# Kernel optimization log

Hardware: AMD Instinct MI355X
Metric: run time of the kernel (lower is better)

Reference implementation:

```python
import jax, jax.numpy as jnp
import numpy as np

D_IN = 1024
D_OUT = 1024
B, S = 4, 2048

def setup_inputs() -> dict:
    key = jax.random.key(0)
    ks = jax.random.split(key, 7)
    s_in = 1.0 / np.sqrt(D_IN)
    return {
        "X": jax.random.normal(ks[0], (B, S, D_IN), dtype=jnp.float32),
        "Wq": jax.random.uniform(ks[1], (D_OUT, D_IN), jnp.float32, -s_in, s_in),
        "bq": jax.random.uniform(ks[2], (D_OUT,), jnp.float32, -s_in, s_in),
        "Wk": jax.random.uniform(ks[3], (D_OUT, D_IN), jnp.float32, -s_in, s_in),
        "bk": jax.random.uniform(ks[4], (D_OUT,), jnp.float32, -s_in, s_in),
        "Wv": jax.random.uniform(ks[5], (D_OUT, D_IN), jnp.float32, -s_in, s_in),
        "bv": jax.random.uniform(ks[6], (D_OUT,), jnp.float32, -s_in, s_in),
    }

def reference(X, Wq, bq, Wk, bk, Wv, bv):
    # Linear projections (torch Linear: x @ W.T + b)
    q = X @ Wq.T + bq            # [B, S, D_OUT]
    k = X @ Wk.T + bk
    v = X @ Wv.T + bv
    scores = jnp.einsum("bqd,bkd->bqk", q, k) / jnp.sqrt(jnp.float32(D_OUT))
    seq = scores.shape[-1]
    causal = jnp.tril(jnp.ones((seq, seq), dtype=bool))  # True where allowed
    scores = jnp.where(causal, scores, -jnp.inf)
    attn = jax.nn.softmax(scores, axis=-1)
    return jnp.einsum("bqk,bkd->bqd", attn, v)
```

## Files before the change

kernel.cpp:

```cpp
#include <hip/hip_runtime.h>
#include <hip/hip_bf16.h>


typedef __attribute__((ext_vector_type(8))) short short8;
typedef __attribute__((ext_vector_type(4))) float floatx4;

#define SEQ   2048
#define DMODEL 1024
#define NBATCH 4
#define MTOT  (SEQ * NBATCH)

__device__ __forceinline__ void stage16(const __hip_bfloat16* g, __hip_bfloat16* l)
{
  __builtin_amdgcn_global_load_lds(
      (const __attribute__((address_space(1))) void*)g,
      (__attribute__((address_space(3))) void*)l, 16, 0, 0);
}

__device__ __forceinline__ unsigned short bf16_bits(float f)
{
  __hip_bfloat16 h = __float2bfloat16(f);
  return *(unsigned short*)&h;
}

__global__ __launch_bounds__(256) void convert_all(
    const float* __restrict__ X,  const float* __restrict__ Wq,
    const float* __restrict__ Wk, const float* __restrict__ Wv,
    __hip_bfloat16* __restrict__ Xb,  __hip_bfloat16* __restrict__ Wqb,
    __hip_bfloat16* __restrict__ Wkb, __hip_bfloat16* __restrict__ Wvb)
{
  const int b = blockIdx.x;
  const float* src; __hip_bfloat16* dst; int rel;
  if (b < 8192)       { src = X;  dst = Xb;  rel = b; }
  else if (b < 9216)  { src = Wq; dst = Wqb; rel = b - 8192; }
  else if (b < 10240) { src = Wk; dst = Wkb; rel = b - 9216; }
  else                { src = Wv; dst = Wvb; rel = b - 10240; }
  const int i = rel * 1024 + threadIdx.x * 4;
  float4 f = *(const float4*)(src + i);
  uint2 o;
  o.x = (unsigned)bf16_bits(f.x) | ((unsigned)bf16_bits(f.y) << 16);
  o.y = (unsigned)bf16_bits(f.z) | ((unsigned)bf16_bits(f.w) << 16);
  *(uint2*)(dst + i) = o;
}

__global__ __launch_bounds__(256, 2) void gemm_qkv_fused(
    const __hip_bfloat16* __restrict__ Xb,
    const __hip_bfloat16* __restrict__ Wqb,
    const __hip_bfloat16* __restrict__ Wkb,
    const __hip_bfloat16* __restrict__ Wvb,
    const float* __restrict__ bq, const float* __restrict__ bk, const float* __restrict__ bv,
    __hip_bfloat16* __restrict__ Qb, __hip_bfloat16* __restrict__ Kb, __hip_bfloat16* __restrict__ Vt)
{
  __shared__ __hip_bfloat16 As[128 * 32];
  __shared__ __hip_bfloat16 Bs[3][128 * 32];
  const int m0 = blockIdx.y * 128, n0 = blockIdx.x * 128;
  const int tid  = threadIdx.x;
  const int lane = tid & 63;
  const int wave = tid >> 6;
  const int quad = lane >> 4;
  const int r    = lane & 15;
  const int wm   = (wave >> 1) * 64;
  const int wn   = (wave & 1) * 64;
  const int srow = wave * 16 + (lane >> 2);
  const int scol = (lane & 3) * 8;

  const __hip_bfloat16* Wp[3] = {Wqb, Wkb, Wvb};

  __hip_bfloat16* lA0 = As + wave * 512;
  __hip_bfloat16* lA1 = As + 2048 + wave * 512;

  const __hip_bfloat16* aR0 = Xb + (size_t)(m0 + srow) * DMODEL + scol;
  const __hip_bfloat16* aR1 = aR0 + (size_t)64 * DMODEL;

  floatx4 acc[3][4][4] = {};

  for (int kt = 0; kt < DMODEL / 32; ++kt) {
    const int k0 = kt * 32;
    stage16(aR0 + k0, lA0);
    stage16(aR1 + k0, lA1);
#pragma unroll
    for (int w = 0; w < 3; ++w) {
      stage16(Wp[w] + (size_t)(n0 + srow) * DMODEL + scol + k0,      Bs[w] + wave * 512);
      stage16(Wp[w] + (size_t)(n0 + 64 + srow) * DMODEL + scol + k0, Bs[w] + 2048 + wave * 512);
    }
    __syncthreads();
    short8 a[4];
#pragma unroll
    for (int i = 0; i < 4; ++i)
      a[i] = *(const short8*)(As + (wm + i * 16 + r) * 32 + quad * 8);
#pragma unroll
    for (int w = 0; w < 3; ++w) {
      short8 b[4];
#pragma unroll
      for (int j = 0; j < 4; ++j)
        b[j] = *(const short8*)(Bs[w] + (wn + j * 16 + r) * 32 + quad * 8);
#pragma unroll
      for (int i = 0; i < 4; ++i)
#pragma unroll
        for (int j = 0; j < 4; ++j)
          acc[w][i][j] = __builtin_amdgcn_mfma_f32_16x16x32_bf16(a[i], b[j], acc[w][i][j], 0, 0, 0);
    }
    __syncthreads();
  }

  {
    __hip_bfloat16* Op[2] = {Qb, Kb};
    const float* Bp[2] = {bq, bk};
#pragma unroll
    for (int w = 0; w < 2; ++w) {
      __hip_bfloat16* out = Op[w];
#pragma unroll
      for (int j = 0; j < 4; ++j) {
        const int n = n0 + wn + j * 16 + r;
        const float bb = Bp[w][n];
#pragma unroll
        for (int i = 0; i < 4; ++i) {
          const int mbase = m0 + wm + i * 16 + quad * 4;
#pragma unroll
          for (int e = 0; e < 4; ++e)
            out[(size_t)(mbase + e) * DMODEL + n] = __float2bfloat16(acc[w][i][j][e] + bb);
        }
      }
    }
  }
  {
    const int z    = m0 >> 11;
    const int posb = (m0 & (SEQ - 1)) + wm;
    __hip_bfloat16* vt = Vt + (size_t)z * DMODEL * SEQ;
#pragma unroll
    for (int j = 0; j < 4; ++j) {
      const int n = n0 + wn + j * 16 + r;
      const float bb = bv[n];
#pragma unroll
      for (int i = 0; i < 4; ++i) {
        const int pos = posb + i * 16 + quad * 4;
        unsigned long long pk =
            (unsigned long long)bf16_bits(acc[2][i][j][0] + bb)
          | ((unsigned long long)bf16_bits(acc[2][i][j][1] + bb) << 16)
          | ((unsigned long long)bf16_bits(acc[2][i][j][2] + bb) << 32)
          | ((unsigned long long)bf16_bits(acc[2][i][j][3] + bb) << 48);
        *(unsigned long long*)(vt + (size_t)n * SEQ + pos) = pk;
      }
    }
  }
}

__device__ __forceinline__ void gemm_core_2w(
    const __hip_bfloat16* __restrict__ A,
    const __hip_bfloat16* __restrict__ B,
    int K, int m0, int n0, int kchunks,
    __hip_bfloat16* As , __hip_bfloat16* Bs ,
    floatx4 acc[4][4])
{
  const int tid  = threadIdx.x;
  const int lane = tid & 63;
  const int wave = tid >> 6;
  const int quad = lane >> 4;
  const int r    = lane & 15;
  const int wn   = wave * 64;
  const int lrow = lane >> 2;
  const int lcol = (lane & 3) * 8;

  const __hip_bfloat16* aB = A + (size_t)(m0 + wave * 32 + lrow) * K + lcol;
  const __hip_bfloat16* bB = B + (size_t)(n0 + wave * 64 + lrow) * K + lcol;
  __hip_bfloat16* lA = As + wave * 1024;
  __hip_bfloat16* lB = Bs + wave * 2048;

  for (int kt = 0; kt < kchunks; ++kt) {
    const int k0 = kt * 32;
#pragma unroll
    for (int s = 0; s < 2; ++s)
      stage16(aB + (size_t)(16 * s) * K + k0, lA + s * 512);
#pragma unroll
    for (int s = 0; s < 4; ++s)
      stage16(bB + (size_t)(16 * s) * K + k0, lB + s * 512);
    __syncthreads();
    short8 a[4], b[4];
#pragma unroll
    for (int i = 0; i < 4; ++i) {
      a[i] = *(const short8*)(As + (i * 16 + r) * 32 + quad * 8);
      b[i] = *(const short8*)(Bs + (wn + i * 16 + r) * 32 + quad * 8);
    }
#pragma unroll
    for (int i = 0; i < 4; ++i)
#pragma unroll
      for (int j = 0; j < 4; ++j)
        acc[i][j] = __builtin_amdgcn_mfma_f32_16x16x32_bf16(a[i], b[j], acc[i][j], 0, 0, 0);
    __syncthreads();
  }
}

__global__ __launch_bounds__(128, 4) void gemm_scores(
    const __hip_bfloat16* __restrict__ Qb, const __hip_bfloat16* __restrict__ Kb,
    __hip_bfloat16* __restrict__ Sb, float* __restrict__ lsum)
{
  const int z = blockIdx.y;
  const int L = blockIdx.x;
  int p = (int)((sqrtf(4.0f * (float)L + 1.0f) - 1.0f) * 0.5f);
  while ((p + 1) * (p + 2) <= L) ++p;
  while (p * (p + 1) > L) --p;
  const int o  = L - p * (p + 1);
  const int mt = 2 * p + (o > p ? 1 : 0);
  const int nt = (o > p) ? (o - p - 1) : o;
  const int m0 = mt * 64, n0 = nt * 128;

  __shared__ __hip_bfloat16 As[64 * 32], Bs[128 * 32];
  const __hip_bfloat16* A = Qb + (size_t)z * SEQ * DMODEL;
  const __hip_bfloat16* B = Kb + (size_t)z * SEQ * DMODEL;
  __hip_bfloat16* outp = Sb + (size_t)z * SEQ * SEQ;
  floatx4 acc[4][4] = {};
  gemm_core_2w(A, B, DMODEL, m0, n0, DMODEL / 32, As, Bs, acc);

  const int lane = threadIdx.x & 63, wave = threadIdx.x >> 6;
  const int quad = lane >> 4, r = lane & 15;
  const int wn = wave * 64;
  const float scale = 0.03125f;
#pragma unroll
  for (int i = 0; i < 4; ++i) {
    const int mbase = m0 + i * 16 + quad * 4;
#pragma unroll
    for (int e = 0; e < 4; ++e) {
      const int row = mbase + e;
      float psum = 0.f;
#pragma unroll
      for (int j = 0; j < 4; ++j) {
        const int n = n0 + wn + j * 16 + r;
        const float pv = (n <= row) ? __expf(acc[i][j][e] * scale) : 0.f;
        outp[(size_t)row * SEQ + n] = __float2bfloat16(pv);
        psum += pv;
      }
#pragma unroll
      for (int off = 1; off < 16; off <<= 1) psum += __shfl_xor(psum, off, 64);
      if (r == 0) atomicAdd(&lsum[z * SEQ + row], psum);
    }
  }
}

__global__ __launch_bounds__(128, 4) void gemm_pv(
    const __hip_bfloat16* __restrict__ Sb, const __hip_bfloat16* __restrict__ Vt,
    const float* __restrict__ lsum, float* __restrict__ Out)
{
  __shared__ __hip_bfloat16 As[64 * 32], Bs[128 * 32];
  const int z = blockIdx.z;
  const int mt = (int)gridDim.y - 1 - (int)blockIdx.y;
  const int m0 = mt * 64, n0 = blockIdx.x * 128;
  const __hip_bfloat16* A = Sb + (size_t)z * SEQ * SEQ;
  const __hip_bfloat16* B = Vt + (size_t)z * DMODEL * SEQ;
  float* outp = Out + (size_t)z * SEQ * DMODEL;

  floatx4 acc[4][4] = {};
  const int kchunks = 2 * mt + 2;
  gemm_core_2w(A, B, SEQ, m0, n0, kchunks, As, Bs, acc);

  const int lane = threadIdx.x & 63, wave = threadIdx.x >> 6;
  const int quad = lane >> 4, r = lane & 15;
  const int wn = wave * 64;
#pragma unroll
  for (int i = 0; i < 4; ++i) {
    const int mbase = m0 + i * 16 + quad * 4;
    float inv[4];
#pragma unroll
    for (int e = 0; e < 4; ++e) inv[e] = 1.f / lsum[z * SEQ + mbase + e];
#pragma unroll
    for (int j = 0; j < 4; ++j) {
      const int n = n0 + wn + j * 16 + r;
#pragma unroll
      for (int e = 0; e < 4; ++e)
        outp[(size_t)(mbase + e) * DMODEL + n] = acc[i][j][e] * inv[e];
    }
  }
}

extern "C" void kernel_launch(void* const* d_in, const int* in_sizes, int n_in,
                              void* d_out, int out_size, void* d_ws, size_t ws_size,
                              hipStream_t stream)
{
  const float* X  = (const float*)d_in[0];
  const float* Wq = (const float*)d_in[1];
  const float* bq = (const float*)d_in[2];
  const float* Wk = (const float*)d_in[3];
  const float* bk = (const float*)d_in[4];
  const float* Wv = (const float*)d_in[5];
  const float* bv = (const float*)d_in[6];
  float* Out = (float*)d_out;

  char* ws = (char*)d_ws;
  size_t off = 0;
  auto alloc = [&](size_t bytes) -> void* {
    void* p = ws + off;
    off += (bytes + 255) & ~(size_t)255;
    return p;
  };
  __hip_bfloat16* Xb  = (__hip_bfloat16*)alloc((size_t)MTOT * DMODEL * 2);
  __hip_bfloat16* Wqb = (__hip_bfloat16*)alloc((size_t)DMODEL * DMODEL * 2);
  __hip_bfloat16* Wkb = (__hip_bfloat16*)alloc((size_t)DMODEL * DMODEL * 2);
  __hip_bfloat16* Wvb = (__hip_bfloat16*)alloc((size_t)DMODEL * DMODEL * 2);
  __hip_bfloat16* Qb  = (__hip_bfloat16*)alloc((size_t)MTOT * DMODEL * 2);
  __hip_bfloat16* Kb  = (__hip_bfloat16*)alloc((size_t)MTOT * DMODEL * 2);
  __hip_bfloat16* Vt  = (__hip_bfloat16*)alloc((size_t)MTOT * DMODEL * 2);
  __hip_bfloat16* Sb  = (__hip_bfloat16*)alloc((size_t)NBATCH * SEQ * SEQ * 2);
  float*          lsum = (float*)alloc((size_t)MTOT * 4);
  (void)ws_size; (void)in_sizes; (void)n_in; (void)out_size;

  hipMemsetAsync(lsum, 0, (size_t)MTOT * 4, stream);
  convert_all<<<11264, 256, 0, stream>>>(X, Wq, Wk, Wv, Xb, Wqb, Wkb, Wvb);
  gemm_qkv_fused<<<dim3(DMODEL / 128, MTOT / 128), 256, 0, stream>>>(
      Xb, Wqb, Wkb, Wvb, bq, bk, bv, Qb, Kb, Vt);
  gemm_scores<<<dim3(272, NBATCH), 128, 0, stream>>>(Qb, Kb, Sb, lsum);
  gemm_pv<<<dim3(DMODEL / 128, SEQ / 64, NBATCH), 128, 0, stream>>>(Sb, Vt, lsum, Out);
}
```

Baseline: 254.2 us.

## Compute softmax row sums via ones-MFMA in PV GEMM instead of atomics

Removes the atomic row-sum accumulation, shuffle reduction and lsum memset from the scores kernel. The PV GEMM instead computes each row's normalizer by an extra MFMA of the probability tile against a ones vector. This drops global atomics and a memset launch but adds roughly a quarter more MFMA work in the PV loop, redundantly across output column blocks.

```diff
diff --git a/kernel.cpp b/kernel.cpp
--- a/kernel.cpp
+++ b/kernel.cpp
@@ -145,12 +145,13 @@
   }
 }
 
+template <bool SUMS>
 __device__ __forceinline__ void gemm_core_2w(
     const __hip_bfloat16* __restrict__ A,
     const __hip_bfloat16* __restrict__ B,
     int K, int m0, int n0, int kchunks,
     __hip_bfloat16* As , __hip_bfloat16* Bs ,
-    floatx4 acc[4][4])
+    floatx4 acc[4][4], floatx4 acc_s[4])
 {
   const int tid  = threadIdx.x;
   const int lane = tid & 63;
@@ -161,6 +162,10 @@
   const int lrow = lane >> 2;
   const int lcol = (lane & 3) * 8;
 
+  short8 ones;
+#pragma unroll
+  for (int t = 0; t < 8; ++t) ones[t] = (short)0x3F80;
+
   const __hip_bfloat16* aB = A + (size_t)(m0 + wave * 32 + lrow) * K + lcol;
   const __hip_bfloat16* bB = B + (size_t)(n0 + wave * 64 + lrow) * K + lcol;
   __hip_bfloat16* lA = As + wave * 1024;
@@ -181,6 +186,11 @@
       a[i] = *(const short8*)(As + (i * 16 + r) * 32 + quad * 8);
       b[i] = *(const short8*)(Bs + (wn + i * 16 + r) * 32 + quad * 8);
     }
+    if (SUMS) {
+#pragma unroll
+      for (int i = 0; i < 4; ++i)
+        acc_s[i] = __builtin_amdgcn_mfma_f32_16x16x32_bf16(a[i], ones, acc_s[i], 0, 0, 0);
+    }
 #pragma unroll
     for (int i = 0; i < 4; ++i)
 #pragma unroll
@@ -192,7 +202,7 @@
 
 __global__ __launch_bounds__(128, 4) void gemm_scores(
     const __hip_bfloat16* __restrict__ Qb, const __hip_bfloat16* __restrict__ Kb,
-    __hip_bfloat16* __restrict__ Sb, float* __restrict__ lsum)
+    __hip_bfloat16* __restrict__ Sb)
 {
   const int z = blockIdx.y;
   const int L = blockIdx.x;
@@ -209,7 +219,8 @@
   const __hip_bfloat16* B = Kb + (size_t)z * SEQ * DMODEL;
   __hip_bfloat16* outp = Sb + (size_t)z * SEQ * SEQ;
   floatx4 acc[4][4] = {};
-  gemm_core_2w(A, B, DMODEL, m0, n0, DMODEL / 32, As, Bs, acc);
+  floatx4 dummy[4];
+  gemm_core_2w<false>(A, B, DMODEL, m0, n0, DMODEL / 32, As, Bs, acc, dummy);
 
   const int lane = threadIdx.x & 63, wave = threadIdx.x >> 6;
   const int quad = lane >> 4, r = lane & 15;
@@ -221,24 +232,19 @@
 #pragma unroll
     for (int e = 0; e < 4; ++e) {
       const int row = mbase + e;
-      float psum = 0.f;
 #pragma unroll
       for (int j = 0; j < 4; ++j) {
         const int n = n0 + wn + j * 16 + r;
         const float pv = (n <= row) ? __expf(acc[i][j][e] * scale) : 0.f;
         outp[(size_t)row * SEQ + n] = __float2bfloat16(pv);
-        psum += pv;
       }
-#pragma unroll
-      for (int off = 1; off < 16; off <<= 1) psum += __shfl_xor(psum, off, 64);
-      if (r == 0) atomicAdd(&lsum[z * SEQ + row], psum);
     }
   }
 }
 
 __global__ __launch_bounds__(128, 4) void gemm_pv(
     const __hip_bfloat16* __restrict__ Sb, const __hip_bfloat16* __restrict__ Vt,
-    const float* __restrict__ lsum, float* __restrict__ Out)
+    float* __restrict__ Out)
 {
   __shared__ __hip_bfloat16 As[64 * 32], Bs[128 * 32];
   const int z = blockIdx.z;
@@ -249,8 +255,9 @@
   float* outp = Out + (size_t)z * SEQ * DMODEL;
 
   floatx4 acc[4][4] = {};
+  floatx4 acc_s[4] = {};
   const int kchunks = 2 * mt + 2;
-  gemm_core_2w(A, B, SEQ, m0, n0, kchunks, As, Bs, acc);
+  gemm_core_2w<true>(A, B, SEQ, m0, n0, kchunks, As, Bs, acc, acc_s);
 
   const int lane = threadIdx.x & 63, wave = threadIdx.x >> 6;
   const int quad = lane >> 4, r = lane & 15;
@@ -260,7 +267,7 @@
     const int mbase = m0 + i * 16 + quad * 4;
     float inv[4];
 #pragma unroll
-    for (int e = 0; e < 4; ++e) inv[e] = 1.f / lsum[z * SEQ + mbase + e];
+    for (int e = 0; e < 4; ++e) inv[e] = 1.f / acc_s[i][e];
 #pragma unroll
     for (int j = 0; j < 4; ++j) {
       const int n = n0 + wn + j * 16 + r;
@@ -299,13 +306,11 @@
   __hip_bfloat16* Kb  = (__hip_bfloat16*)alloc((size_t)MTOT * DMODEL * 2);
   __hip_bfloat16* Vt  = (__hip_bfloat16*)alloc((size_t)MTOT * DMODEL * 2);
   __hip_bfloat16* Sb  = (__hip_bfloat16*)alloc((size_t)NBATCH * SEQ * SEQ * 2);
-  float*          lsum = (float*)alloc((size_t)MTOT * 4);
   (void)ws_size; (void)in_sizes; (void)n_in; (void)out_size;
 
-  hipMemsetAsync(lsum, 0, (size_t)MTOT * 4, stream);
   convert_all<<<11264, 256, 0, stream>>>(X, Wq, Wk, Wv, Xb, Wqb, Wkb, Wvb);
   gemm_qkv_fused<<<dim3(DMODEL / 128, MTOT / 128), 256, 0, stream>>>(
       Xb, Wqb, Wkb, Wvb, bq, bk, bv, Qb, Kb, Vt);
-  gemm_scores<<<dim3(272, NBATCH), 128, 0, stream>>>(Qb, Kb, Sb, lsum);
-  gemm_pv<<<dim3(DMODEL / 128, SEQ / 64, NBATCH), 128, 0, stream>>>(Sb, Vt, lsum, Out);
-}
+  gemm_scores<<<dim3(272, NBATCH), 128, 0, stream>>>(Qb, Kb, Sb);
+  gemm_pv<<<dim3(DMODEL / 128, SEQ / 64, NBATCH), 128, 0, stream>>>(Sb, Vt, Out);
+}
```

New measurement: 247.7 us (median of 2 runs). -2.6%, faster.
